# Kernel optimization log

Hardware: AMD Instinct MI355X
Metric: run time of the kernel (lower is better)

## Reference

```python
import jax, jax.numpy as jnp
import numpy as np

# Module config (matches init_kwargs)
N, D1, D2, BW, K = 8, 1024, 1024, 4, 4
D = D1 * D2
B = 4096
TEMPERATURE = 1.0


def setup_inputs() -> dict:
    key = jax.random.key(0)
    ks = jax.random.split(key, 6)
    x = jax.random.normal(ks[0], (B, N, D1), dtype=jnp.float32)
    # learned parameters (kaiming-ish normal init; exact init does not matter for correctness baseline)
    U = jax.random.normal(ks[1], (N, D, K), dtype=jnp.float32)
    V = jax.random.normal(ks[2], (BW, D, K), dtype=jnp.float32)
    scale = jax.random.normal(ks[3], (N, 1), dtype=jnp.float32)
    biasq = jax.random.normal(ks[4], (N, 1), dtype=jnp.float32)
    bias = jax.random.normal(ks[5], (N, D2), dtype=jnp.float32)
    return {"x": x, "U": U, "V": V, "scale": scale, "biasq": biasq, "bias": bias}


def reference(x, U, V, scale, biasq, bias):
    # twopow = [2^0, ..., 2^{bw-1}] (non-learned buffer)
    twopow = 2.0 ** jnp.arange(BW, dtype=jnp.float32)
    # CP contraction: Theta[n, b, d] = sum_k U[n,d,k] * V[b,d,k]
    Theta = jnp.einsum('ndk,bdk->nbd', U, V)  # (N, BW, D)
    # sigmoid with temperature T, input clamped to [-10, 10]
    soft_binary = jax.nn.sigmoid(jnp.clip(TEMPERATURE * Theta, -10.0, 10.0))
    # bit-weighted sum -> soft integer per weight element
    integer = jnp.einsum('nbd,b->nd', soft_binary, twopow)  # (N, D)
    # dequantize: scale * (integer - biasq - 2^bw)
    w = scale * (integer - biasq - 2.0 ** BW)  # (N, D)
    w = w.reshape(N, D1, D2)
    # batched per-ensemble-member GEMM: act[b,n,l] = sum_d x[b,n,d] * w[n,d,l]
    act = jnp.einsum('bnd,ndl->bnl', x, w) + bias  # bias broadcasts (N, D2)
    return act
```

## Files before the change

kernel.cpp:

```cpp
#include <hip/hip_runtime.h>
#include <hip/hip_bf16.h>


typedef __attribute__((ext_vector_type(8))) short short8;
typedef __attribute__((ext_vector_type(4))) float f32x4;
typedef __attribute__((ext_vector_type(4))) unsigned short ushort4v;
typedef __attribute__((ext_vector_type(2))) unsigned int uint2v;

__device__ __forceinline__ unsigned short f2bf(float f) {
  union { float f; unsigned u; } a; a.f = f;
  unsigned u = a.u;
  u += 0x7fffu + ((u >> 16) & 1u);
  return (unsigned short)(u >> 16);
}

__device__ __forceinline__ unsigned pk2(float a, float b) {
  __hip_bfloat162 h = __float22bfloat162_rn(make_float2(a, b));
  union { __hip_bfloat162 h; unsigned u; } c; c.h = h;
  return c.u;
}

__global__ __launch_bounds__(256) void wgen_kernel(
    const float4* __restrict__ U4, const float4* __restrict__ V4,
    const float* __restrict__ scale, const float* __restrict__ biasq,
    unsigned short* __restrict__ Wt) {
  __shared__ float tiles[8][32][33];
  const int t = threadIdx.x;
  const int d1_0 = blockIdx.x * 32;
  const int d2_0 = blockIdx.y * 32;
#pragma unroll
  for (int i = 0; i < 4; i++) {
    const int e = t + 256 * i;
    const int r = e >> 5, c = e & 31;
    const size_t d = (size_t)(d1_0 + r) * 1024 + (size_t)(d2_0 + c);
    float4 u[8];
#pragma unroll
    for (int nn = 0; nn < 8; nn++) u[nn] = U4[((size_t)nn << 20) + d];
    float integ[8];
#pragma unroll
    for (int nn = 0; nn < 8; nn++) integ[nn] = 0.f;
#pragma unroll
    for (int b = 0; b < 4; b++) {
      const float4 v = V4[((size_t)b << 20) + d];
      const float pw = (float)(1 << b);
#pragma unroll
      for (int nn = 0; nn < 8; nn++) {
        float th = u[nn].x * v.x + u[nn].y * v.y + u[nn].z * v.z + u[nn].w * v.w;
        th = fminf(10.f, fmaxf(-10.f, th));
        integ[nn] += pw * __builtin_amdgcn_rcpf(1.f + __expf(-th));
      }
    }
#pragma unroll
    for (int nn = 0; nn < 8; nn++) tiles[nn][r][c] = integ[nn];
  }
  __syncthreads();
  const int orow = t >> 3;
  const int oc0 = (t & 7) * 4;
#pragma unroll
  for (int nn = 0; nn < 8; nn++) {
    const float sc = scale[nn], bq = biasq[nn];
    ushort4v o;
    o.x = f2bf(sc * (tiles[nn][oc0 + 0][orow] - bq - 16.f));
    o.y = f2bf(sc * (tiles[nn][oc0 + 1][orow] - bq - 16.f));
    o.z = f2bf(sc * (tiles[nn][oc0 + 2][orow] - bq - 16.f));
    o.w = f2bf(sc * (tiles[nn][oc0 + 3][orow] - bq - 16.f));
    *(ushort4v*)(Wt + ((size_t)nn << 20) + (size_t)(d2_0 + orow) * 1024 +
                 (size_t)(d1_0 + oc0)) = o;
  }
}

__global__ __launch_bounds__(256) void xcast_kernel(
    const float4* __restrict__ X4, uint2v* __restrict__ Xb) {
  const size_t total = (size_t)4096 * 8 * 1024 / 4;
  const size_t stride = (size_t)gridDim.x * 256;
  for (size_t i = (size_t)blockIdx.x * 256 + threadIdx.x; i < total; i += stride) {
    const float4 v = X4[i];
    uint2v p;
    p.x = pk2(v.x, v.y);
    p.y = pk2(v.z, v.w);
    Xb[i] = p;
  }
}

#define AS1(p) ((const __attribute__((address_space(1))) void*)(p))
#define AS3(p) ((__attribute__((address_space(3))) void*)(p))

__global__ __launch_bounds__(256) void gemm_kernel(
    const unsigned short* __restrict__ Xb,
    const unsigned short* __restrict__ Wt,
    const float* __restrict__ bias,
    float* __restrict__ out) {
  __shared__ unsigned short As[128 * 64];
  __shared__ unsigned short Bs[128 * 64];
  const int t = threadIdx.x;
  const int wv = t >> 6;
  const int ln = t & 63;

  const int lin = (int)(blockIdx.x + 32u * blockIdx.y + 256u * blockIdx.z);
  const int g   = (lin & 7) | ((lin >> 6) << 3);
  const int bnb = (lin >> 3) & 7;
  const int n   = g >> 5;
  const int bm0 = (g & 31) * 128;
  const int bn0 = bnb * 128;

  const int sr = wv * 8 + (ln >> 3);
  const int sc = (((ln & 7) ^ (sr & 7)) * 8);
  const unsigned short* ag =
      Xb + ((size_t)(bm0 + sr) * 8 + (size_t)n) * 1024 + sc;
  const unsigned short* bg =
      Wt + ((size_t)n << 20) + (size_t)(bn0 + sr) * 1024 + sc;
  unsigned short* lA = As + wv * 512;
  unsigned short* lB = Bs + wv * 512;

  const int wm = wv >> 1, wn = wv & 1;
  const int lm = ln & 15;
  const int cq = ln >> 4;
  const int sw = lm & 7;
  const unsigned short* a_rd = As + (wm * 64 + lm) * 64;
  const unsigned short* b_rd = Bs + (wn * 64 + lm) * 64;

  f32x4 acc[4][4];
#pragma unroll
  for (int i = 0; i < 4; i++)
#pragma unroll
    for (int j = 0; j < 4; j++) acc[i][j] = (f32x4){0.f, 0.f, 0.f, 0.f};

  for (int k0 = 0; k0 < 1024; k0 += 64) {
#pragma unroll
    for (int r = 0; r < 4; r++)
      __builtin_amdgcn_global_load_lds(AS1(ag + (size_t)(32 * r) * 8192 + k0),
                                       AS3(lA + r * 2048), 16, 0, 0);
#pragma unroll
    for (int r = 0; r < 4; r++)
      __builtin_amdgcn_global_load_lds(AS1(bg + (size_t)(32 * r) * 1024 + k0),
                                       AS3(lB + r * 2048), 16, 0, 0);
    __syncthreads();
#pragma unroll
    for (int half = 0; half < 2; half++) {
      const int off = ((half * 4 + cq) ^ sw) * 8;
      short8 af[4], bfr[4];
#pragma unroll
      for (int i = 0; i < 4; i++) af[i] = *(const short8*)(a_rd + i * 1024 + off);
#pragma unroll
      for (int j = 0; j < 4; j++) bfr[j] = *(const short8*)(b_rd + j * 1024 + off);
#pragma unroll
      for (int i = 0; i < 4; i++)
#pragma unroll
        for (int j = 0; j < 4; j++)
          acc[i][j] = __builtin_amdgcn_mfma_f32_16x16x32_bf16(af[i], bfr[j],
                                                              acc[i][j], 0, 0, 0);
    }
    __syncthreads();
  }

  const int q = ln >> 4;
  const int row0 = bm0 + wm * 64 + q * 4;
  const int col0 = bn0 + wn * 64 + lm;
  float bv[4];
#pragma unroll
  for (int j = 0; j < 4; j++) bv[j] = bias[n * 1024 + col0 + j * 16];
#pragma unroll
  for (int i = 0; i < 4; i++) {
#pragma unroll
    for (int r = 0; r < 4; r++) {
      const int row = row0 + i * 16 + r;
      float* op = out + ((size_t)row * 8 + (size_t)n) * 1024;
#pragma unroll
      for (int j = 0; j < 4; j++) op[col0 + j * 16] = acc[i][j][r] + bv[j];
    }
  }
}

extern "C" void kernel_launch(void* const* d_in, const int* in_sizes, int n_in,
                              void* d_out, int out_size, void* d_ws, size_t ws_size,
                              hipStream_t stream) {
  const float* x     = (const float*)d_in[0];
  const float* U     = (const float*)d_in[1];
  const float* V     = (const float*)d_in[2];
  const float* scale = (const float*)d_in[3];
  const float* biasq = (const float*)d_in[4];
  const float* bias  = (const float*)d_in[5];
  float* out = (float*)d_out;

  unsigned short* Wt = (unsigned short*)d_ws;
  unsigned short* Xb = (unsigned short*)d_ws + (size_t)8 * 1024 * 1024;

  wgen_kernel<<<dim3(32, 32), 256, 0, stream>>>((const float4*)U, (const float4*)V,
                                                scale, biasq, Wt);
  xcast_kernel<<<dim3(2048), 256, 0, stream>>>((const float4*)x, (uint2v*)Xb);
  gemm_kernel<<<dim3(32, 8, 8), 256, 0, stream>>>(Xb, Wt, bias, out);
}
```

Before: 467.8 us.

## Merge prep kernels and rewrite GEMM with 256x256 double-buffered pipelined tiles

Fuses the weight-generation and x-cast kernels into one launch, with blocks split by index, to save a launch and let both run concurrently. Rewrites the GEMM to use 256x256 tiles with 8 waves and double-buffered LDS. Direct global-to-LDS loads for the next k-tile are interleaved with four MFMA phases using explicit vmcnt waits, barriers and setprio. The larger tiles and 128 accumulators per lane raise register and LDS pressure, and the hand-placed waitcnt ordering is fragile.

```diff
diff --git a/kernel.cpp b/kernel.cpp
--- a/kernel.cpp
+++ b/kernel.cpp
@@ -20,153 +20,198 @@
   return c.u;
 }
 
-__global__ __launch_bounds__(256) void wgen_kernel(
+__global__ __launch_bounds__(256) void prep_kernel(
     const float4* __restrict__ U4, const float4* __restrict__ V4,
     const float* __restrict__ scale, const float* __restrict__ biasq,
-    unsigned short* __restrict__ Wt) {
+    unsigned short* __restrict__ Wt,
+    const float4* __restrict__ X4, uint2v* __restrict__ Xb) {
   __shared__ float tiles[8][32][33];
+  const int bid = blockIdx.x;
   const int t = threadIdx.x;
-  const int d1_0 = blockIdx.x * 32;
-  const int d2_0 = blockIdx.y * 32;
-#pragma unroll
-  for (int i = 0; i < 4; i++) {
-    const int e = t + 256 * i;
-    const int r = e >> 5, c = e & 31;
-    const size_t d = (size_t)(d1_0 + r) * 1024 + (size_t)(d2_0 + c);
-    float4 u[8];
-#pragma unroll
-    for (int nn = 0; nn < 8; nn++) u[nn] = U4[((size_t)nn << 20) + d];
-    float integ[8];
-#pragma unroll
-    for (int nn = 0; nn < 8; nn++) integ[nn] = 0.f;
-#pragma unroll
-    for (int b = 0; b < 4; b++) {
-      const float4 v = V4[((size_t)b << 20) + d];
-      const float pw = (float)(1 << b);
-#pragma unroll
-      for (int nn = 0; nn < 8; nn++) {
-        float th = u[nn].x * v.x + u[nn].y * v.y + u[nn].z * v.z + u[nn].w * v.w;
-        th = fminf(10.f, fmaxf(-10.f, th));
-        integ[nn] += pw * __builtin_amdgcn_rcpf(1.f + __expf(-th));
+  if (bid < 1024) {
+    const int d1_0 = (bid & 31) * 32;
+    const int d2_0 = (bid >> 5) * 32;
+#pragma unroll
+    for (int i = 0; i < 4; i++) {
+      const int e = t + 256 * i;
+      const int r = e >> 5, c = e & 31;
+      const size_t d = (size_t)(d1_0 + r) * 1024 + (size_t)(d2_0 + c);
+      float4 u[8];
+#pragma unroll
+      for (int nn = 0; nn < 8; nn++) u[nn] = U4[((size_t)nn << 20) + d];
+      float integ[8];
+#pragma unroll
+      for (int nn = 0; nn < 8; nn++) integ[nn] = 0.f;
+#pragma unroll
+      for (int b = 0; b < 4; b++) {
+        const float4 v = V4[((size_t)b << 20) + d];
+        const float pw = (float)(1 << b);
+#pragma unroll
+        for (int nn = 0; nn < 8; nn++) {
+          float th = u[nn].x * v.x + u[nn].y * v.y + u[nn].z * v.z + u[nn].w * v.w;
+          th = fminf(10.f, fmaxf(-10.f, th));
+          integ[nn] += pw * __builtin_amdgcn_rcpf(1.f + __expf(-th));
+        }
       }
-    }
-#pragma unroll
-    for (int nn = 0; nn < 8; nn++) tiles[nn][r][c] = integ[nn];
-  }
-  __syncthreads();
-  const int orow = t >> 3;
-  const int oc0 = (t & 7) * 4;
-#pragma unroll
-  for (int nn = 0; nn < 8; nn++) {
-    const float sc = scale[nn], bq = biasq[nn];
-    ushort4v o;
-    o.x = f2bf(sc * (tiles[nn][oc0 + 0][orow] - bq - 16.f));
-    o.y = f2bf(sc * (tiles[nn][oc0 + 1][orow] - bq - 16.f));
-    o.z = f2bf(sc * (tiles[nn][oc0 + 2][orow] - bq - 16.f));
-    o.w = f2bf(sc * (tiles[nn][oc0 + 3][orow] - bq - 16.f));
-    *(ushort4v*)(Wt + ((size_t)nn << 20) + (size_t)(d2_0 + orow) * 1024 +
-                 (size_t)(d1_0 + oc0)) = o;
-  }
-}
-
-__global__ __launch_bounds__(256) void xcast_kernel(
-    const float4* __restrict__ X4, uint2v* __restrict__ Xb) {
-  const size_t total = (size_t)4096 * 8 * 1024 / 4;
-  const size_t stride = (size_t)gridDim.x * 256;
-  for (size_t i = (size_t)blockIdx.x * 256 + threadIdx.x; i < total; i += stride) {
-    const float4 v = X4[i];
-    uint2v p;
-    p.x = pk2(v.x, v.y);
-    p.y = pk2(v.z, v.w);
-    Xb[i] = p;
+#pragma unroll
+      for (int nn = 0; nn < 8; nn++) tiles[nn][r][c] = integ[nn];
+    }
+    __syncthreads();
+    const int orow = t >> 3;
+    const int oc0 = (t & 7) * 4;
+#pragma unroll
+    for (int nn = 0; nn < 8; nn++) {
+      const float sc = scale[nn], bq = biasq[nn];
+      ushort4v o;
+      o.x = f2bf(sc * (tiles[nn][oc0 + 0][orow] - bq - 16.f));
+      o.y = f2bf(sc * (tiles[nn][oc0 + 1][orow] - bq - 16.f));
+      o.z = f2bf(sc * (tiles[nn][oc0 + 2][orow] - bq - 16.f));
+      o.w = f2bf(sc * (tiles[nn][oc0 + 3][orow] - bq - 16.f));
+      *(ushort4v*)(Wt + ((size_t)nn << 20) + (size_t)(d2_0 + orow) * 1024 +
+                   (size_t)(d1_0 + oc0)) = o;
+    }
+  } else {
+    const size_t total = (size_t)4096 * 8 * 1024 / 4;
+    const size_t stride = (size_t)2048 * 256;
+    for (size_t i = (size_t)(bid - 1024) * 256 + t; i < total; i += stride) {
+      const float4 v = X4[i];
+      uint2v p;
+      p.x = pk2(v.x, v.y);
+      p.y = pk2(v.z, v.w);
+      Xb[i] = p;
+    }
   }
 }
 
 #define AS1(p) ((const __attribute__((address_space(1))) void*)(p))
 #define AS3(p) ((__attribute__((address_space(3))) void*)(p))
 
-__global__ __launch_bounds__(256) void gemm_kernel(
+#define PHASE(mq, nq, STAGE)                                                   \
+  {                                                                            \
+    __builtin_amdgcn_s_barrier();                                              \
+    __builtin_amdgcn_sched_barrier(0);                                         \
+    short8 af[4][2], bfv[2][2];                                                \
+    _Pragma("unroll")                                                          \
+    for (int mf2 = 0; mf2 < 4; mf2++)                                          \
+      _Pragma("unroll")                                                        \
+      for (int ks = 0; ks < 2; ks++)                                           \
+        af[mf2][ks] = *(const short8*)(aRd + db16 + (mq) * 8192 +              \
+                                       mf2 * 2048 + ks * 32 + cq8);            \
+    _Pragma("unroll")                                                          \
+    for (int nf2 = 0; nf2 < 2; nf2++)                                          \
+      _Pragma("unroll")                                                        \
+      for (int ks = 0; ks < 2; ks++)                                           \
+        bfv[nf2][ks] = *(const short8*)(bRd + db16 + (nq) * 8192 +             \
+                                        nf2 * 4096 + ks * 32 + cq8);           \
+    STAGE;                                                                     \
+    __builtin_amdgcn_s_setprio(1);                                             \
+    _Pragma("unroll")                                                          \
+    for (int ks = 0; ks < 2; ks++)                                             \
+      _Pragma("unroll")                                                        \
+      for (int mf2 = 0; mf2 < 4; mf2++)                                        \
+        _Pragma("unroll")                                                      \
+        for (int nf2 = 0; nf2 < 2; nf2++)                                      \
+          acc[(mq) * 4 + mf2][(nq) * 2 + nf2] =                                \
+              __builtin_amdgcn_mfma_f32_16x16x32_bf16(                         \
+                  af[mf2][ks], bfv[nf2][ks],                                   \
+                  acc[(mq) * 4 + mf2][(nq) * 2 + nf2], 0, 0, 0);               \
+    __builtin_amdgcn_s_setprio(0);                                             \
+  }
+
+__global__ __launch_bounds__(512, 2) void gemm_kernel(
     const unsigned short* __restrict__ Xb,
     const unsigned short* __restrict__ Wt,
     const float* __restrict__ bias,
     float* __restrict__ out) {
-  __shared__ unsigned short As[128 * 64];
-  __shared__ unsigned short Bs[128 * 64];
+  __shared__ unsigned short As[2 * 256 * 64];
+  __shared__ unsigned short Bs[2 * 256 * 64];
   const int t = threadIdx.x;
-  const int wv = t >> 6;
+  const int w = t >> 6;
   const int ln = t & 63;
-
-  const int lin = (int)(blockIdx.x + 32u * blockIdx.y + 256u * blockIdx.z);
-  const int g   = (lin & 7) | ((lin >> 6) << 3);
-  const int bnb = (lin >> 3) & 7;
-  const int n   = g >> 5;
-  const int bm0 = (g & 31) * 128;
-  const int bn0 = bnb * 128;
-
-  const int sr = wv * 8 + (ln >> 3);
-  const int sc = (((ln & 7) ^ (sr & 7)) * 8);
-  const unsigned short* ag =
-      Xb + ((size_t)(bm0 + sr) * 8 + (size_t)n) * 1024 + sc;
-  const unsigned short* bg =
-      Wt + ((size_t)n << 20) + (size_t)(bn0 + sr) * 1024 + sc;
-  unsigned short* lA = As + wv * 512;
-  unsigned short* lB = Bs + wv * 512;
-
-  const int wm = wv >> 1, wn = wv & 1;
+  const int wm = w >> 2;
+  const int wn = w & 3;
+
+  const int lin = blockIdx.x;
+  const int n   = lin & 7;
+  const int bn0 = ((lin >> 3) & 3) * 256;
+  const int bm0 = (lin >> 5) * 256;
+
+  const int s_r = ln >> 3;
+  const int s_c = (ln & 7) ^ (((ln >> 5) & 1) << 1);
+  const unsigned short* aB =
+      Xb + ((size_t)(bm0 + w * 16 + s_r) * 8 + n) * 1024 + s_c * 8;
+  const unsigned short* bB =
+      Wt + ((size_t)n << 20) + (size_t)(bn0 + w * 16 + s_r) * 1024 + s_c * 8;
+  unsigned short* aL = As + w * 1024;
+  unsigned short* bL = Bs + w * 1024;
+
+  auto stageA = [&](int dbuf, int h, int kt) {
+#pragma unroll
+    for (int l = 0; l < 2; l++)
+      __builtin_amdgcn_global_load_lds(
+          AS1(aB + (size_t)h * 1048576 + (size_t)l * 65536 + kt * 64),
+          AS3(aL + dbuf * 16384 + h * 8192 + l * 512), 16, 0, 0);
+  };
+  auto stageB = [&](int dbuf, int h, int kt) {
+#pragma unroll
+    for (int l = 0; l < 2; l++)
+      __builtin_amdgcn_global_load_lds(
+          AS1(bB + (size_t)h * 131072 + (size_t)l * 8192 + kt * 64),
+          AS3(bL + dbuf * 16384 + h * 8192 + l * 512), 16, 0, 0);
+  };
+
   const int lm = ln & 15;
-  const int cq = ln >> 4;
-  const int sw = lm & 7;
-  const unsigned short* a_rd = As + (wm * 64 + lm) * 64;
-  const unsigned short* b_rd = Bs + (wn * 64 + lm) * 64;
-
-  f32x4 acc[4][4];
-#pragma unroll
-  for (int i = 0; i < 4; i++)
+  const int kq = ln >> 4;
+  const int cq8 = (kq ^ (((lm >> 2) & 1) << 1)) * 8;
+  const unsigned short* aRd = As + (wm * 16 + lm) * 64;
+  const unsigned short* bRd = Bs + (wn * 16 + lm) * 64;
+
+  f32x4 acc[8][4];
+#pragma unroll
+  for (int i = 0; i < 8; i++)
 #pragma unroll
     for (int j = 0; j < 4; j++) acc[i][j] = (f32x4){0.f, 0.f, 0.f, 0.f};
 
-  for (int k0 = 0; k0 < 1024; k0 += 64) {
-#pragma unroll
-    for (int r = 0; r < 4; r++)
-      __builtin_amdgcn_global_load_lds(AS1(ag + (size_t)(32 * r) * 8192 + k0),
-                                       AS3(lA + r * 2048), 16, 0, 0);
-#pragma unroll
-    for (int r = 0; r < 4; r++)
-      __builtin_amdgcn_global_load_lds(AS1(bg + (size_t)(32 * r) * 1024 + k0),
-                                       AS3(lB + r * 2048), 16, 0, 0);
-    __syncthreads();
-#pragma unroll
-    for (int half = 0; half < 2; half++) {
-      const int off = ((half * 4 + cq) ^ sw) * 8;
-      short8 af[4], bfr[4];
-#pragma unroll
-      for (int i = 0; i < 4; i++) af[i] = *(const short8*)(a_rd + i * 1024 + off);
-#pragma unroll
-      for (int j = 0; j < 4; j++) bfr[j] = *(const short8*)(b_rd + j * 1024 + off);
-#pragma unroll
-      for (int i = 0; i < 4; i++)
-#pragma unroll
-        for (int j = 0; j < 4; j++)
-          acc[i][j] = __builtin_amdgcn_mfma_f32_16x16x32_bf16(af[i], bfr[j],
-                                                              acc[i][j], 0, 0, 0);
-    }
-    __syncthreads();
-  }
-
-  const int q = ln >> 4;
-  const int row0 = bm0 + wm * 64 + q * 4;
-  const int col0 = bn0 + wn * 64 + lm;
+  stageA(0, 0, 0); stageB(0, 0, 0); stageB(0, 1, 0); stageA(0, 1, 0);
+
+  for (int kt = 0; kt < 15; kt++) {
+    const int db16 = (kt & 1) * 16384;
+    const int nb = (kt & 1) ^ 1;
+    const int nkt = kt + 1;
+    asm volatile("s_waitcnt vmcnt(4)" ::: "memory");
+    PHASE(0, 0, stageA(nb, 0, nkt));
+    asm volatile("s_waitcnt vmcnt(4)" ::: "memory");
+    PHASE(0, 1, stageB(nb, 0, nkt));
+    asm volatile("s_waitcnt vmcnt(4)" ::: "memory");
+    PHASE(1, 0, stageB(nb, 1, nkt));
+    PHASE(1, 1, stageA(nb, 1, nkt));
+  }
+  {
+    const int db16 = 16384;
+    asm volatile("s_waitcnt vmcnt(4)" ::: "memory");
+    PHASE(0, 0, (void)0);
+    asm volatile("s_waitcnt vmcnt(2)" ::: "memory");
+    PHASE(0, 1, (void)0);
+    asm volatile("s_waitcnt vmcnt(0)" ::: "memory");
+    PHASE(1, 0, (void)0);
+    PHASE(1, 1, (void)0);
+  }
+
+  const int q4 = ln >> 4;
   float bv[4];
 #pragma unroll
-  for (int j = 0; j < 4; j++) bv[j] = bias[n * 1024 + col0 + j * 16];
-#pragma unroll
-  for (int i = 0; i < 4; i++) {
+  for (int nf = 0; nf < 4; nf++)
+    bv[nf] = bias[n * 1024 + bn0 + (nf >> 1) * 128 + (nf & 1) * 64 + wn * 16 + lm];
+#pragma unroll
+  for (int mf = 0; mf < 8; mf++) {
+    const int rowb = bm0 + (mf >> 2) * 128 + (mf & 3) * 32 + wm * 16 + q4 * 4;
 #pragma unroll
     for (int r = 0; r < 4; r++) {
-      const int row = row0 + i * 16 + r;
-      float* op = out + ((size_t)row * 8 + (size_t)n) * 1024;
-#pragma unroll
-      for (int j = 0; j < 4; j++) op[col0 + j * 16] = acc[i][j][r] + bv[j];
+      float* op = out + ((size_t)(rowb + r) * 8 + n) * 1024;
+#pragma unroll
+      for (int nf = 0; nf < 4; nf++)
+        op[bn0 + (nf >> 1) * 128 + (nf & 1) * 64 + wn * 16 + lm] =
+            acc[mf][nf][r] + bv[nf];
     }
   }
 }
@@ -185,8 +230,8 @@
   unsigned short* Wt = (unsigned short*)d_ws;
   unsigned short* Xb = (unsigned short*)d_ws + (size_t)8 * 1024 * 1024;
 
-  wgen_kernel<<<dim3(32, 32), 256, 0, stream>>>((const float4*)U, (const float4*)V,
-                                                scale, biasq, Wt);
-  xcast_kernel<<<dim3(2048), 256, 0, stream>>>((const float4*)x, (uint2v*)Xb);
-  gemm_kernel<<<dim3(32, 8, 8), 256, 0, stream>>>(Xb, Wt, bias, out);
-}
+  prep_kernel<<<dim3(3072), 256, 0, stream>>>((const float4*)U, (const float4*)V,
+                                              scale, biasq, Wt,
+                                              (const float4*)x, (uint2v*)Xb);
+  gemm_kernel<<<dim3(512), 512, 0, stream>>>(Xb, Wt, bias, out);
+}
```

New measurement: 470.6 us. No clear change (+0.6%).
